# Kernel tuning notes

Measured on AMD Instinct MI355X. Metric: run time of the kernel, lower is better.

Reference implementation:

```python
import jax, jax.numpy as jnp
import numpy as np

FP8_MAX = 448.0  # max normal of float8_e4m3fn (TE fwd format)
EPS = 1e-12


def _fp8_quant_dequant(t):
    """Per-tensor amax scaling -> cast to e4m3 -> dequant back to f32.
    Mirrors TE's per-tensor scaling recipe (scale = FP8_MAX / amax)."""
    amax = jnp.max(jnp.abs(t))
    scale = FP8_MAX / jnp.maximum(amax, EPS)
    q = jnp.clip(t * scale, -FP8_MAX, FP8_MAX).astype(jnp.float8_e4m3fn)
    return q.astype(jnp.float32) / scale


def setup_inputs() -> dict:
    key = jax.random.key(0)
    k1, k2, k3 = jax.random.split(key, 3)
    tokens, d_in, d_out = 8192, 4096, 4096
    x = jax.random.normal(k1, (tokens, d_in), dtype=jnp.float32)
    # kaiming_uniform_(a=sqrt(5)) -> U(-bound, bound), bound = sqrt(6/((1+a^2)*fan_in)) = 1/sqrt(fan_in)
    bound = 1.0 / np.sqrt(d_in)
    weight = jax.random.uniform(k2, (d_out, d_in), dtype=jnp.float32, minval=-bound, maxval=bound)
    bias = jnp.zeros((d_out,), dtype=jnp.float32) + 0.01 * jax.random.normal(k3, (d_out,), dtype=jnp.float32)
    return {"x": x, "weight": weight, "bias": bias}


def reference(x, weight, bias):
    # fp8 quant/dequant of activations and weights, then GEMM + bias
    xq = _fp8_quant_dequant(x)            # [T, Din]
    wq = _fp8_quant_dequant(weight)       # [Dout, Din]
    out = jnp.einsum("ti,oi->to", xq, wq) # [T, Dout]
    return out + bias[None, :]
```

## Files before the change

kernel.cpp:

```cpp
#include <hip/hip_runtime.h>
#include <stdint.h>

#define M_DIM 8192
#define N_DIM 4096
#define K_DIM 4096

typedef float f32x4 __attribute__((ext_vector_type(4)));
typedef int   i32x4 __attribute__((ext_vector_type(4)));
typedef int   i32x8 __attribute__((ext_vector_type(8)));

__global__ void init_ws_kernel(unsigned int* ws_u) {
    ws_u[0] = 0u;
    ws_u[1] = 0u;
}

__global__ __launch_bounds__(256) void amax_kernel(const float* __restrict__ in,
                                                   int n4,
                                                   unsigned int* __restrict__ target) {
    int tid = blockIdx.x * blockDim.x + threadIdx.x;
    int stride = gridDim.x * blockDim.x;
    const float4* p = (const float4*)in;
    float m = 0.0f;
    for (int i = tid; i < n4; i += stride) {
        float4 v = p[i];
        m = fmaxf(m, fmaxf(fmaxf(fabsf(v.x), fabsf(v.y)),
                           fmaxf(fabsf(v.z), fabsf(v.w))));
    }
#pragma unroll
    for (int off = 32; off > 0; off >>= 1)
        m = fmaxf(m, __shfl_down(m, off, 64));
    __shared__ float sm[4];
    if ((threadIdx.x & 63) == 0) sm[threadIdx.x >> 6] = m;
    __syncthreads();
    if (threadIdx.x == 0) {
        m = fmaxf(fmaxf(sm[0], sm[1]), fmaxf(sm[2], sm[3]));
        atomicMax(target, __float_as_uint(m));
    }
}

__global__ __launch_bounds__(256) void quant_kernel(const float* __restrict__ in,
                                                    unsigned int* __restrict__ outp,
                                                    int n4,
                                                    const unsigned int* __restrict__ ws_u,
                                                    int slot) {
    float amax = fmaxf(__uint_as_float(ws_u[slot]), 1e-12f);
    float scale = 448.0f / amax;
    int tid = blockIdx.x * blockDim.x + threadIdx.x;
    int stride = gridDim.x * blockDim.x;
    const float4* p = (const float4*)in;
    for (int i = tid; i < n4; i += stride) {
        float4 v = p[i];
        float a = fminf(fmaxf(v.x * scale, -448.0f), 448.0f);
        float b = fminf(fmaxf(v.y * scale, -448.0f), 448.0f);
        float c = fminf(fmaxf(v.z * scale, -448.0f), 448.0f);
        float d = fminf(fmaxf(v.w * scale, -448.0f), 448.0f);
        int w = __builtin_amdgcn_cvt_pk_fp8_f32(a, b, 0, false);
        w = __builtin_amdgcn_cvt_pk_fp8_f32(c, d, w, true);
        outp[i] = (unsigned int)w;
    }
}

__device__ __forceinline__ void gld16(const void* g, void* l) {
    __builtin_amdgcn_global_load_lds(
        (const __attribute__((address_space(1))) void*)g,
        (__attribute__((address_space(3))) void*)l, 16, 0, 0);
}

#define MFMA_MX(a, b, c) __builtin_amdgcn_mfma_scale_f32_16x16x128_f8f6f4( \
    (a), (b), (c), 0, 0, 0, 0x7F7F7F7F, 0, 0x7F7F7F7F)

__global__ __launch_bounds__(512, 2) void gemm_fp8_kernel(
    const uint8_t* __restrict__ Aq,
    const uint8_t* __restrict__ Bq,
    const float* __restrict__ bias,
    const unsigned int* __restrict__ ws_u,
    float* __restrict__ out)
{
    __shared__ uint8_t lds[131072];

    const int tid = threadIdx.x;
    const int w = tid >> 6, l = tid & 63;

    const int cpx = (int)gridDim.x >> 3;
    const int bid = (int)blockIdx.x;
    const int swz = (bid & 7) * cpx + (bid >> 3);
    const int bm = swz >> 4, bn = swz & 15;

    const uint8_t* gA = Aq + (size_t)bm * 256 * K_DIM;
    const uint8_t* gB = Bq + (size_t)bn * 256 * K_DIM;

    const int idx = tid >> 3, p = tid & 7;
    const int rB = (idx & 31) + ((idx >> 5) << 6);
    const int srcX = ((p ^ (idx & 7)) << 4);
    const int dA = tid * 16;
    const int dB = tid * 16 + ((tid >> 8) << 12);

    const int wr = w >> 2, wc = w & 3;
    const int lr = l & 15, g = l >> 4;
    const int oLo = (((2 * g) ^ (lr & 7)) << 4);
    const int oHi = (((2 * g + 1) ^ (lr & 7)) << 4);
    const int rowA0 = wr * 128 + lr;
    const int rowB0 = wc * 64 + lr;

    auto stA = [&](int bb, const uint8_t* gsrc, int rbase) {
        const int row = idx + rbase;
        gld16(gsrc + (size_t)row * K_DIM + srcX,
              &lds[bb * 32768 + rbase * 128 + dA]);
    };
    auto stB = [&](int bb, const uint8_t* gsrc, int boff, int r) {
        const int row = rB + boff + (r << 7);
        gld16(gsrc + (size_t)row * K_DIM + srcX,
              &lds[65536 + bb * 32768 + (boff << 7) + (r << 14) + dB]);
    };
    auto ldf = [&](const uint8_t* base, int row) -> i32x8 {
        const uint8_t* q = base + (row << 7);
        i32x4 lo = *(const i32x4*)(q + oLo);
        i32x4 hi = *(const i32x4*)(q + oHi);
        return __builtin_shufflevector(lo, hi, 0, 1, 2, 3, 4, 5, 6, 7);
    };

    f32x4 acc[8][4] = {};
    i32x8 av[4], bv[4];

    stA(0, gA, 0);   stA(0, gA, 128);
    stB(0, gB, 0, 0); stB(0, gB, 0, 1);
    stA(0, gA, 64);  stA(0, gA, 192);
    stB(0, gB, 32, 0); stB(0, gB, 32, 1);

    for (int t = 0; t < 31; ++t) {
        const int buf = t & 1, nbuf = buf ^ 1;
        const uint8_t* gAn = gA + (size_t)(t + 1) * 128;
        const uint8_t* gBn = gB + (size_t)(t + 1) * 128;
        const uint8_t* lab = &lds[buf * 32768];
        const uint8_t* lbb = &lds[65536 + buf * 32768];

        asm volatile("s_waitcnt vmcnt(4)" ::: "memory");
        __builtin_amdgcn_s_barrier();
        stA(nbuf, gAn, 0); stA(nbuf, gAn, 128);
        av[0] = ldf(lab, rowA0);      av[1] = ldf(lab, rowA0 + 16);
        av[2] = ldf(lab, rowA0 + 32); av[3] = ldf(lab, rowA0 + 48);
        bv[0] = ldf(lbb, rowB0);      bv[1] = ldf(lbb, rowB0 + 16);
        __builtin_amdgcn_s_setprio(1);
        acc[0][0] = MFMA_MX(av[0], bv[0], acc[0][0]);
        acc[0][1] = MFMA_MX(av[0], bv[1], acc[0][1]);
        acc[1][0] = MFMA_MX(av[1], bv[0], acc[1][0]);
        acc[1][1] = MFMA_MX(av[1], bv[1], acc[1][1]);
        acc[2][0] = MFMA_MX(av[2], bv[0], acc[2][0]);
        acc[2][1] = MFMA_MX(av[2], bv[1], acc[2][1]);
        acc[3][0] = MFMA_MX(av[3], bv[0], acc[3][0]);
        acc[3][1] = MFMA_MX(av[3], bv[1], acc[3][1]);
        __builtin_amdgcn_s_setprio(0);

        asm volatile("s_waitcnt vmcnt(2)" ::: "memory");
        __builtin_amdgcn_s_barrier();
        stB(nbuf, gBn, 0, 0); stB(nbuf, gBn, 0, 1);
        bv[2] = ldf(lbb, rowB0 + 32); bv[3] = ldf(lbb, rowB0 + 48);
        __builtin_amdgcn_s_setprio(1);
        acc[0][2] = MFMA_MX(av[0], bv[2], acc[0][2]);
        acc[0][3] = MFMA_MX(av[0], bv[3], acc[0][3]);
        acc[1][2] = MFMA_MX(av[1], bv[2], acc[1][2]);
        acc[1][3] = MFMA_MX(av[1], bv[3], acc[1][3]);
        acc[2][2] = MFMA_MX(av[2], bv[2], acc[2][2]);
        acc[2][3] = MFMA_MX(av[2], bv[3], acc[2][3]);
        acc[3][2] = MFMA_MX(av[3], bv[2], acc[3][2]);
        acc[3][3] = MFMA_MX(av[3], bv[3], acc[3][3]);
        __builtin_amdgcn_s_setprio(0);

        stA(nbuf, gAn, 64); stA(nbuf, gAn, 192);
        av[0] = ldf(lab, rowA0 + 64); av[1] = ldf(lab, rowA0 + 80);
        av[2] = ldf(lab, rowA0 + 96); av[3] = ldf(lab, rowA0 + 112);
        __builtin_amdgcn_s_setprio(1);
        acc[4][0] = MFMA_MX(av[0], bv[0], acc[4][0]);
        acc[4][1] = MFMA_MX(av[0], bv[1], acc[4][1]);
        acc[5][0] = MFMA_MX(av[1], bv[0], acc[5][0]);
        acc[5][1] = MFMA_MX(av[1], bv[1], acc[5][1]);
        acc[6][0] = MFMA_MX(av[2], bv[0], acc[6][0]);
        acc[6][1] = MFMA_MX(av[2], bv[1], acc[6][1]);
        acc[7][0] = MFMA_MX(av[3], bv[0], acc[7][0]);
        acc[7][1] = MFMA_MX(av[3], bv[1], acc[7][1]);
        __builtin_amdgcn_s_setprio(0);

        stB(nbuf, gBn, 32, 0); stB(nbuf, gBn, 32, 1);
        __builtin_amdgcn_s_setprio(1);
        acc[4][2] = MFMA_MX(av[0], bv[2], acc[4][2]);
        acc[4][3] = MFMA_MX(av[0], bv[3], acc[4][3]);
        acc[5][2] = MFMA_MX(av[1], bv[2], acc[5][2]);
        acc[5][3] = MFMA_MX(av[1], bv[3], acc[5][3]);
        acc[6][2] = MFMA_MX(av[2], bv[2], acc[6][2]);
        acc[6][3] = MFMA_MX(av[2], bv[3], acc[6][3]);
        acc[7][2] = MFMA_MX(av[3], bv[2], acc[7][2]);
        acc[7][3] = MFMA_MX(av[3], bv[3], acc[7][3]);
        __builtin_amdgcn_s_setprio(0);
    }

    {
        const uint8_t* lab = &lds[32768];
        const uint8_t* lbb = &lds[65536 + 32768];

        asm volatile("s_waitcnt vmcnt(4)" ::: "memory");
        __builtin_amdgcn_s_barrier();
        av[0] = ldf(lab, rowA0);      av[1] = ldf(lab, rowA0 + 16);
        av[2] = ldf(lab, rowA0 + 32); av[3] = ldf(lab, rowA0 + 48);
        bv[0] = ldf(lbb, rowB0);      bv[1] = ldf(lbb, rowB0 + 16);
#pragma unroll
        for (int m = 0; m < 4; ++m) {
            acc[m][0] = MFMA_MX(av[m], bv[0], acc[m][0]);
            acc[m][1] = MFMA_MX(av[m], bv[1], acc[m][1]);
        }
        asm volatile("s_waitcnt vmcnt(0)" ::: "memory");
        __builtin_amdgcn_s_barrier();
        bv[2] = ldf(lbb, rowB0 + 32); bv[3] = ldf(lbb, rowB0 + 48);
#pragma unroll
        for (int m = 0; m < 4; ++m) {
            acc[m][2] = MFMA_MX(av[m], bv[2], acc[m][2]);
            acc[m][3] = MFMA_MX(av[m], bv[3], acc[m][3]);
        }
        av[0] = ldf(lab, rowA0 + 64); av[1] = ldf(lab, rowA0 + 80);
        av[2] = ldf(lab, rowA0 + 96); av[3] = ldf(lab, rowA0 + 112);
#pragma unroll
        for (int m = 0; m < 4; ++m) {
            acc[4 + m][0] = MFMA_MX(av[m], bv[0], acc[4 + m][0]);
            acc[4 + m][1] = MFMA_MX(av[m], bv[1], acc[4 + m][1]);
            acc[4 + m][2] = MFMA_MX(av[m], bv[2], acc[4 + m][2]);
            acc[4 + m][3] = MFMA_MX(av[m], bv[3], acc[4 + m][3]);
        }
    }

    const float ax = fmaxf(__uint_as_float(ws_u[0]), 1e-12f);
    const float aw = fmaxf(__uint_as_float(ws_u[1]), 1e-12f);
    const float inv = (ax * (1.0f / 448.0f)) * (aw * (1.0f / 448.0f));

    const int orow0 = bm * 256 + wr * 128 + g * 4;
    const int ocol0 = bn * 256 + wc * 64 + lr;
#pragma unroll
    for (int mb = 0; mb < 8; ++mb) {
#pragma unroll
        for (int nb = 0; nb < 4; ++nb) {
            const int col = ocol0 + nb * 16;
            const float bvv = bias[col];
#pragma unroll
            for (int j = 0; j < 4; ++j) {
                const int row = orow0 + mb * 16 + j;
                out[(size_t)row * N_DIM + col] = acc[mb][nb][j] * inv + bvv;
            }
        }
    }
}

extern "C" void kernel_launch(void* const* d_in, const int* in_sizes, int n_in,
                              void* d_out, int out_size, void* d_ws, size_t ws_size,
                              hipStream_t stream) {
    const float* x    = (const float*)d_in[0];
    const float* wgt  = (const float*)d_in[1];
    const float* bias = (const float*)d_in[2];
    float* out = (float*)d_out;

    unsigned int* ws_u = (unsigned int*)d_ws;
    uint8_t* xq = (uint8_t*)d_ws + 256;
    uint8_t* wq = xq + (size_t)M_DIM * K_DIM;

    init_ws_kernel<<<1, 1, 0, stream>>>(ws_u);
    amax_kernel<<<1024, 256, 0, stream>>>(x,   M_DIM * K_DIM / 4, ws_u + 0);
    amax_kernel<<<1024, 256, 0, stream>>>(wgt, N_DIM * K_DIM / 4, ws_u + 1);
    quant_kernel<<<2048, 256, 0, stream>>>(x,   (unsigned int*)xq, M_DIM * K_DIM / 4, ws_u, 0);
    quant_kernel<<<2048, 256, 0, stream>>>(wgt, (unsigned int*)wq, N_DIM * K_DIM / 4, ws_u, 1);

    gemm_fp8_kernel<<<(M_DIM / 256) * (N_DIM / 256), 512, 0, stream>>>(
        xq, wq, bias, ws_u, out);
}
```

Before: 219.5 us.

## Merge amax/quant launches and restructure GEMM barrier and LDS-load schedule

Merges the paired amax and quant kernels into single 2-D grid launches, one for x and one for the weight, and replaces the init kernel with a memset. This cuts launch count and lets both tensors be processed concurrently. The GEMM main loop is also reordered: LDS fragment reads are issued before the global-to-LDS prefetches, extra barriers and lgkmcnt waits are added around each MFMA phase, and global addressing uses precomputed row pointers. The added barriers may increase synchronisation stalls. The edit bv[3 - 1] is equivalent to bv[2] and changes nothing.

```diff
diff --git a/kernel.cpp b/kernel.cpp
--- a/kernel.cpp
+++ b/kernel.cpp
@@ -9,17 +9,14 @@
 typedef int   i32x4 __attribute__((ext_vector_type(4)));
 typedef int   i32x8 __attribute__((ext_vector_type(8)));
 
-__global__ void init_ws_kernel(unsigned int* ws_u) {
-    ws_u[0] = 0u;
-    ws_u[1] = 0u;
-}
-
-__global__ __launch_bounds__(256) void amax_kernel(const float* __restrict__ in,
-                                                   int n4,
-                                                   unsigned int* __restrict__ target) {
+__global__ __launch_bounds__(256) void amax2_kernel(const float* __restrict__ x,
+                                                    const float* __restrict__ wgt,
+                                                    unsigned int* __restrict__ ws_u) {
+    const int which = blockIdx.y;
+    const float4* p = (const float4*)(which ? wgt : x);
+    const int n4 = (which ? N_DIM : M_DIM) * (K_DIM / 4);
     int tid = blockIdx.x * blockDim.x + threadIdx.x;
     int stride = gridDim.x * blockDim.x;
-    const float4* p = (const float4*)in;
     float m = 0.0f;
     for (int i = tid; i < n4; i += stride) {
         float4 v = p[i];
@@ -34,20 +31,23 @@
     __syncthreads();
     if (threadIdx.x == 0) {
         m = fmaxf(fmaxf(sm[0], sm[1]), fmaxf(sm[2], sm[3]));
-        atomicMax(target, __float_as_uint(m));
-    }
-}
-
-__global__ __launch_bounds__(256) void quant_kernel(const float* __restrict__ in,
-                                                    unsigned int* __restrict__ outp,
-                                                    int n4,
-                                                    const unsigned int* __restrict__ ws_u,
-                                                    int slot) {
-    float amax = fmaxf(__uint_as_float(ws_u[slot]), 1e-12f);
+        atomicMax(ws_u + which, __float_as_uint(m));
+    }
+}
+
+__global__ __launch_bounds__(256) void quant2_kernel(const float* __restrict__ x,
+                                                     const float* __restrict__ wgt,
+                                                     unsigned int* __restrict__ xq,
+                                                     unsigned int* __restrict__ wq,
+                                                     const unsigned int* __restrict__ ws_u) {
+    const int which = blockIdx.y;
+    const float4* p = (const float4*)(which ? wgt : x);
+    unsigned int* outp = which ? wq : xq;
+    const int n4 = (which ? N_DIM : M_DIM) * (K_DIM / 4);
+    float amax = fmaxf(__uint_as_float(ws_u[which]), 1e-12f);
     float scale = 448.0f / amax;
     int tid = blockIdx.x * blockDim.x + threadIdx.x;
     int stride = gridDim.x * blockDim.x;
-    const float4* p = (const float4*)in;
     for (int i = tid; i < n4; i += stride) {
         float4 v = p[i];
         float a = fminf(fmaxf(v.x * scale, -448.0f), 448.0f);
@@ -68,6 +68,11 @@
 
 #define MFMA_MX(a, b, c) __builtin_amdgcn_mfma_scale_f32_16x16x128_f8f6f4( \
     (a), (b), (c), 0, 0, 0, 0x7F7F7F7F, 0, 0x7F7F7F7F)
+#define BAR()    __builtin_amdgcn_s_barrier()
+#define LGKM0()  asm volatile("s_waitcnt lgkmcnt(0)" ::: "memory")
+#define VMCNT(n) asm volatile("s_waitcnt vmcnt(" #n ")" ::: "memory")
+#define PRIO1()  __builtin_amdgcn_s_setprio(1)
+#define PRIO0()  __builtin_amdgcn_s_setprio(0)
 
 __global__ __launch_bounds__(512, 2) void gemm_fp8_kernel(
     const uint8_t* __restrict__ Aq,
@@ -90,8 +95,10 @@
     const uint8_t* gB = Bq + (size_t)bn * 256 * K_DIM;
 
     const int idx = tid >> 3, p = tid & 7;
+    const int srcX = ((p ^ (idx & 7)) << 4);
     const int rB = (idx & 31) + ((idx >> 5) << 6);
-    const int srcX = ((p ^ (idx & 7)) << 4);
+    const uint8_t* aRow = gA + (size_t)idx * K_DIM + srcX;
+    const uint8_t* bRow = gB + (size_t)rB * K_DIM + srcX;
     const int dA = tid * 16;
     const int dB = tid * 16 + ((tid >> 8) << 12);
 
@@ -102,14 +109,12 @@
     const int rowA0 = wr * 128 + lr;
     const int rowB0 = wc * 64 + lr;
 
-    auto stA = [&](int bb, const uint8_t* gsrc, int rbase) {
-        const int row = idx + rbase;
-        gld16(gsrc + (size_t)row * K_DIM + srcX,
+    auto stA = [&](int bb, int kn, int rbase) {
+        gld16(aRow + (size_t)rbase * K_DIM + kn,
               &lds[bb * 32768 + rbase * 128 + dA]);
     };
-    auto stB = [&](int bb, const uint8_t* gsrc, int boff, int r) {
-        const int row = rB + boff + (r << 7);
-        gld16(gsrc + (size_t)row * K_DIM + srcX,
+    auto stB = [&](int bb, int kn, int boff, int r) {
+        gld16(bRow + (size_t)(boff + (r << 7)) * K_DIM + kn,
               &lds[65536 + bb * 32768 + (boff << 7) + (r << 14) + dB]);
     };
     auto ldf = [&](const uint8_t* base, int row) -> i32x8 {
@@ -122,25 +127,24 @@
     f32x4 acc[8][4] = {};
     i32x8 av[4], bv[4];
 
-    stA(0, gA, 0);   stA(0, gA, 128);
-    stB(0, gB, 0, 0); stB(0, gB, 0, 1);
-    stA(0, gA, 64);  stA(0, gA, 192);
-    stB(0, gB, 32, 0); stB(0, gB, 32, 1);
+    stA(0, 0, 0);    stA(0, 0, 128);
+    stB(0, 0, 0, 0); stB(0, 0, 0, 1);
+    stA(0, 0, 64);   stA(0, 0, 192);
+    stB(0, 0, 32, 0); stB(0, 0, 32, 1);
+    VMCNT(4); BAR();
 
     for (int t = 0; t < 31; ++t) {
         const int buf = t & 1, nbuf = buf ^ 1;
-        const uint8_t* gAn = gA + (size_t)(t + 1) * 128;
-        const uint8_t* gBn = gB + (size_t)(t + 1) * 128;
+        const int kn = (t + 1) * 128;
         const uint8_t* lab = &lds[buf * 32768];
         const uint8_t* lbb = &lds[65536 + buf * 32768];
 
-        asm volatile("s_waitcnt vmcnt(4)" ::: "memory");
-        __builtin_amdgcn_s_barrier();
-        stA(nbuf, gAn, 0); stA(nbuf, gAn, 128);
         av[0] = ldf(lab, rowA0);      av[1] = ldf(lab, rowA0 + 16);
         av[2] = ldf(lab, rowA0 + 32); av[3] = ldf(lab, rowA0 + 48);
         bv[0] = ldf(lbb, rowB0);      bv[1] = ldf(lbb, rowB0 + 16);
-        __builtin_amdgcn_s_setprio(1);
+        stA(nbuf, kn, 0); stA(nbuf, kn, 128);
+        BAR(); LGKM0();
+        PRIO1();
         acc[0][0] = MFMA_MX(av[0], bv[0], acc[0][0]);
         acc[0][1] = MFMA_MX(av[0], bv[1], acc[0][1]);
         acc[1][0] = MFMA_MX(av[1], bv[0], acc[1][0]);
@@ -149,13 +153,14 @@
         acc[2][1] = MFMA_MX(av[2], bv[1], acc[2][1]);
         acc[3][0] = MFMA_MX(av[3], bv[0], acc[3][0]);
         acc[3][1] = MFMA_MX(av[3], bv[1], acc[3][1]);
-        __builtin_amdgcn_s_setprio(0);
-
-        asm volatile("s_waitcnt vmcnt(2)" ::: "memory");
-        __builtin_amdgcn_s_barrier();
-        stB(nbuf, gBn, 0, 0); stB(nbuf, gBn, 0, 1);
+        PRIO0();
+        VMCNT(2);
+        BAR();
+
         bv[2] = ldf(lbb, rowB0 + 32); bv[3] = ldf(lbb, rowB0 + 48);
-        __builtin_amdgcn_s_setprio(1);
+        stB(nbuf, kn, 0, 0); stB(nbuf, kn, 0, 1);
+        BAR(); LGKM0();
+        PRIO1();
         acc[0][2] = MFMA_MX(av[0], bv[2], acc[0][2]);
         acc[0][3] = MFMA_MX(av[0], bv[3], acc[0][3]);
         acc[1][2] = MFMA_MX(av[1], bv[2], acc[1][2]);
@@ -164,12 +169,14 @@
         acc[2][3] = MFMA_MX(av[2], bv[3], acc[2][3]);
         acc[3][2] = MFMA_MX(av[3], bv[2], acc[3][2]);
         acc[3][3] = MFMA_MX(av[3], bv[3], acc[3][3]);
-        __builtin_amdgcn_s_setprio(0);
-
-        stA(nbuf, gAn, 64); stA(nbuf, gAn, 192);
+        PRIO0();
+        BAR();
+
         av[0] = ldf(lab, rowA0 + 64); av[1] = ldf(lab, rowA0 + 80);
         av[2] = ldf(lab, rowA0 + 96); av[3] = ldf(lab, rowA0 + 112);
-        __builtin_amdgcn_s_setprio(1);
+        stA(nbuf, kn, 64); stA(nbuf, kn, 192);
+        BAR(); LGKM0();
+        PRIO1();
         acc[4][0] = MFMA_MX(av[0], bv[0], acc[4][0]);
         acc[4][1] = MFMA_MX(av[0], bv[1], acc[4][1]);
         acc[5][0] = MFMA_MX(av[1], bv[0], acc[5][0]);
@@ -178,27 +185,29 @@
         acc[6][1] = MFMA_MX(av[2], bv[1], acc[6][1]);
         acc[7][0] = MFMA_MX(av[3], bv[0], acc[7][0]);
         acc[7][1] = MFMA_MX(av[3], bv[1], acc[7][1]);
-        __builtin_amdgcn_s_setprio(0);
-
-        stB(nbuf, gBn, 32, 0); stB(nbuf, gBn, 32, 1);
-        __builtin_amdgcn_s_setprio(1);
+        PRIO0();
+        BAR();
+
+        stB(nbuf, kn, 32, 0); stB(nbuf, kn, 32, 1);
+        BAR();
+        PRIO1();
         acc[4][2] = MFMA_MX(av[0], bv[2], acc[4][2]);
         acc[4][3] = MFMA_MX(av[0], bv[3], acc[4][3]);
         acc[5][2] = MFMA_MX(av[1], bv[2], acc[5][2]);
         acc[5][3] = MFMA_MX(av[1], bv[3], acc[5][3]);
         acc[6][2] = MFMA_MX(av[2], bv[2], acc[6][2]);
         acc[6][3] = MFMA_MX(av[2], bv[3], acc[6][3]);
-        acc[7][2] = MFMA_MX(av[3], bv[2], acc[7][2]);
+        acc[7][2] = MFMA_MX(av[3], bv[3 - 1], acc[7][2]);
         acc[7][3] = MFMA_MX(av[3], bv[3], acc[7][3]);
-        __builtin_amdgcn_s_setprio(0);
+        PRIO0();
+        VMCNT(4);
+        BAR();
     }
 
     {
         const uint8_t* lab = &lds[32768];
         const uint8_t* lbb = &lds[65536 + 32768];
 
-        asm volatile("s_waitcnt vmcnt(4)" ::: "memory");
-        __builtin_amdgcn_s_barrier();
         av[0] = ldf(lab, rowA0);      av[1] = ldf(lab, rowA0 + 16);
         av[2] = ldf(lab, rowA0 + 32); av[3] = ldf(lab, rowA0 + 48);
         bv[0] = ldf(lbb, rowB0);      bv[1] = ldf(lbb, rowB0 + 16);
@@ -207,8 +216,7 @@
             acc[m][0] = MFMA_MX(av[m], bv[0], acc[m][0]);
             acc[m][1] = MFMA_MX(av[m], bv[1], acc[m][1]);
         }
-        asm volatile("s_waitcnt vmcnt(0)" ::: "memory");
-        __builtin_amdgcn_s_barrier();
+        VMCNT(0); BAR();
         bv[2] = ldf(lbb, rowB0 + 32); bv[3] = ldf(lbb, rowB0 + 48);
 #pragma unroll
         for (int m = 0; m < 4; ++m) {
@@ -259,11 +267,14 @@
     uint8_t* xq = (uint8_t*)d_ws + 256;
     uint8_t* wq = xq + (size_t)M_DIM * K_DIM;
 
-    init_ws_kernel<<<1, 1, 0, stream>>>(ws_u);
-    amax_kernel<<<1024, 256, 0, stream>>>(x,   M_DIM * K_DIM / 4, ws_u + 0);
-    amax_kernel<<<1024, 256, 0, stream>>>(wgt, N_DIM * K_DIM / 4, ws_u + 1);
-    quant_kernel<<<2048, 256, 0, stream>>>(x,   (unsigned int*)xq, M_DIM * K_DIM / 4, ws_u, 0);
-    quant_kernel<<<2048, 256, 0, stream>>>(wgt, (unsigned int*)wq, N_DIM * K_DIM / 4, ws_u, 1);
+    hipMemsetAsync(d_ws, 0, 8, stream);
+
+    dim3 ga(1024, 2);
+    amax2_kernel<<<ga, 256, 0, stream>>>(x, wgt, ws_u);
+
+    dim3 gq(2048, 2);
+    quant2_kernel<<<gq, 256, 0, stream>>>(x, wgt, (unsigned int*)xq,
+                                          (unsigned int*)wq, ws_u);
 
     gemm_fp8_kernel<<<(M_DIM / 256) * (N_DIM / 256), 512, 0, stream>>>(
         xq, wq, bias, ws_u, out);
```

New measurement: 221.4 us. Within noise of the previous version (+0.9%).
